# Kernel optimization log

Hardware: AMD Instinct MI355X
Metric: run time of the kernel (lower is better)

The kernel has to match this reference:

```python
import jax, jax.numpy as jnp
import numpy as np

N_U = 16        # walkers per molecule
N_ORB = 12      # number of orbitals
N_FEAT = 14     # feature dim, fixed by w being 14x14
H1_THR = 0.0
H2_THR = 0.0


def setup_inputs() -> dict:
    key = jax.random.key(0)
    k1, k2, k3, k4, k5 = jax.random.split(key, 5)
    B = 16
    T = B * N_U  # 256 total walker samples
    mfv = jax.random.normal(k1, (T, N_ORB, N_FEAT), jnp.float32) * 0.1
    h1 = jax.random.normal(k2, (T, N_ORB, N_ORB), jnp.float32)
    h2 = jax.random.normal(k3, (T, N_ORB, N_ORB, N_ORB, N_ORB), jnp.float32)
    # occupancies in {1,2} so p_x_i determinants are generically nonzero
    V_n_hf = 1 + jax.random.randint(k4, (B, N_U, N_ORB), 0, 2, jnp.int32)
    w = jax.random.normal(k5, (N_FEAT, N_FEAT), jnp.float32) * 0.1
    return {"molec_feature_vectors": mfv, "h1": h1, "h2": h2,
            "V_n_hf": V_n_hf, "w": w}


def _forward(mfv, h1, h2, V_n_hf, w):
    T, n, f = mfv.shape
    B = T // N_U
    Vn = V_n_hf.reshape(T, n)                      # (T, n_orb) int occupancies

    eye = jnp.eye(n, dtype=jnp.int32)
    # c^dag c excitation patterns: (n, n^2)
    c1 = (eye[:, None, :] - eye[:, :, None]).reshape(n, n * n)
    # c^dag c^dag c c patterns: (n, n^4)
    c2 = (c1[:, None, :] - c1[:, :, None]).reshape(n, n ** 4)
    Wsym = w + w.T
    h1f = h1.reshape(T, n * n)
    h2f = h2.reshape(T, n ** 4)

    def per_sample(x, h1v, h2v, phi):
        # G[a,i] = phi[a] @ Wsym @ phi[i]; the c-sum inside calc_ampl factors as
        # det( G * (S S^T) ) because einsum('abc,bj,ijc->aic') keeps c aligned.
        G = phi @ Wsym @ phi.T                     # (n, n)

        # ---- one-body term ----
        s1 = c1 + x[:, None]                       # (n, n^2)
        m1 = ((s1.max(0) - s1.min(0)) == 1) & (h1v > H1_THR)
        s1f = s1.astype(phi.dtype) * m1            # boolean_mask -> zero columns
        det1 = jnp.linalg.det(G * (s1f @ s1f.T))
        e1 = det1 ** 2 * jnp.sum(jnp.where(m1, h1v, 0.0) ** 2)

        # ---- two-body term ----
        s2 = c2 + x[:, None]                       # (n, n^4)
        m2 = ((s2.max(0) - s2.min(0)) == 1) & (h2v > H2_THR)
        s2f = s2.astype(phi.dtype) * m2
        # reduce_sum over (orbital, feature) of phi[:, :, None] * s2[:, None, :]
        a2 = phi.sum(1) @ s2f                      # (n^4,)
        e2 = jnp.sum((jnp.where(m2, h2v, 0.0) * a2) ** 2)

        # ---- sampling probability of current state ----
        xf = x.astype(phi.dtype)
        p = jnp.linalg.det(G * jnp.outer(xf, xf)) ** 2
        return e1 + e2, p

    e, p = jax.vmap(per_sample)(Vn, h1f, h2f, mfv)
    e = e.reshape(B, N_U)
    p = p.reshape(B, N_U)
    return jnp.sum(e * p, axis=1) / jnp.sum(p, axis=1)   # (B,)


def reference(molec_feature_vectors, h1, h2, V_n_hf, w):
    return _forward(molec_feature_vectors, h1, h2, V_n_hf, w)
```

## Files before the change

kernel.cpp:

```cpp
#include <hip/hip_runtime.h>

#define NORB   12
#define NFEAT  14
#define NCOL1  144
#define NCOL2  20736
#define RPB    192
#define NSPLIT 9
#define CPS    (NSPLIT + 1)
#define NT     256
#define WPS    (NSPLIT * 3)

extern "C" __global__ void __launch_bounds__(RPB)
eloc_fused(const float* __restrict__ mfv, const float* __restrict__ h1,
           const float* __restrict__ h2, const int* __restrict__ vn,
           const float* __restrict__ w,
           double* __restrict__ ep, double* __restrict__ part)
{
    const int tid = threadIdx.x;
    const int bid = blockIdx.x;
    const int t   = bid / CPS;
    const int ch  = bid % CPS;

    __shared__ float phi_s[NORB][NFEAT];
    __shared__ int   x_s[NORB];
    __shared__ float W_s[NFEAT][NFEAT];
    __shared__ float tmp_s[NORB][NFEAT];
    __shared__ float G_s[NORB][NORB];
    __shared__ unsigned char m1_s[NCOL1];
    __shared__ int Ri_s[NORB], Rj_s[NORB], M_s;
    __shared__ double A1[NORB][NORB], A2[NORB][NORB];
    __shared__ double red_s[RPB / 64];
    __shared__ double det_s[2];
    __shared__ double h1sum_s;

    if (ch != 0) {
        const int lane = tid & 63, wvi = tid >> 6;
        const int r = (ch - 1) * RPB + tid;
        const int i = r / 144, j = (r / NORB) % NORB, p = r % NORB;

        const float4* hr = (const float4*)(h2 + (size_t)t * NCOL2 + (size_t)r * NORB);
        const float4 ha = hr[0], hb = hr[1], hc = hr[2];

        int   xv  = 1;
        float psl = 0.f;
        if (lane < NORB) {
            xv = vn[t * NORB + lane];
            const float* pr = mfv + (size_t)t * NORB * NFEAT + lane * NFEAT;
            float s = 0.f;
            #pragma unroll
            for (int f = 0; f < NFEAT; ++f) s += pr[f];
            psl = s;
        }
        const unsigned long long bal = __ballot(xv == 2);
        const int X2  = (int)(bal & 0xFFFull);
        const int nx2 = ~X2 & 0xFFF;

        float sv = (lane < NORB) ? psl * (float)xv : 0.f;
        sv += __shfl_xor(sv, 8, 16);
        sv += __shfl_xor(sv, 4, 16);
        sv += __shfl_xor(sv, 2, 16);
        sv += __shfl_xor(sv, 1, 16);
        const float Sv = __shfl(sv, 0, 64);

        float psv[NORB];
        #pragma unroll
        for (int q = 0; q < NORB; ++q) psv[q] = __shfl(psl, q, 64);

        const int bi = 1 << i, bj = 1 << j, bp = 1 << p;
        const int um0 = 0xFFF & ~(bi | bj | bp);
        const int xi = 1 + ((X2 >> i) & 1);
        const int xj = 1 + ((X2 >> j) & 1);
        const int xp = 1 + ((X2 >> p) & 1);
        const int basei = xi + 1 - ((bi >> j) & 1) - ((bi >> p) & 1);
        const int basej = xj + ((bj >> i) & 1) - 1 - ((bj >> p) & 1);
        const int basep = xp + ((bp >> i) & 1) - ((bp >> j) & 1) - 1;
        const float a2b = Sv + __shfl(psl, i, 64) - __shfl(psl, j, 64)
                        - __shfl(psl, p, 64);

        float acc = 0.f;
#define COLQ(q, hv) {                                                       \
        const int bq  = 1 << (q);                                           \
        const int um  = um0 & ~bq;                                          \
        const int hm1 = nx2 & um, hm2 = X2 & um;                            \
        int mn = hm1 ? 1 : (hm2 ? 2 : 9);                                   \
        int mx = hm2 ? 2 : (hm1 ? 1 : -9);                                  \
        const int iq = (bi >> (q)) & 1, jq = (bj >> (q)) & 1,               \
                  pq = (bp >> (q)) & 1;                                     \
        const int vi = basei + iq, vj = basej + jq, vp = basep + pq;        \
        const int xq = 1 + ((X2 >> (q)) & 1);                               \
        const int vq = xq + 1 + iq - jq - pq;                               \
        mn = min(min(mn, vi), min(vj, min(vp, vq)));                        \
        mx = max(max(mx, vi), max(vj, max(vp, vq)));                        \
        const bool ok = (mx - mn == 1) && ((hv) > 0.0f);                    \
        const float tq = ok ? (hv) * (a2b + psv[q]) : 0.0f;                 \
        acc = fmaf(tq, tq, acc);                                            \
    }
        COLQ(0,  ha.x)  COLQ(1,  ha.y)  COLQ(2,  ha.z)  COLQ(3,  ha.w)
        COLQ(4,  hb.x)  COLQ(5,  hb.y)  COLQ(6,  hb.z)  COLQ(7,  hb.w)
        COLQ(8,  hc.x)  COLQ(9,  hc.y)  COLQ(10, hc.z)  COLQ(11, hc.w)
#undef COLQ

        double accd = (double)acc;
        #pragma unroll
        for (int o = 32; o > 0; o >>= 1) accd += __shfl_down(accd, o, 64);
        if (lane == 0) part[t * WPS + (ch - 1) * 3 + wvi] = accd;
    } else {
        if (tid < NORB * NFEAT)
            phi_s[tid / NFEAT][tid % NFEAT] = mfv[(size_t)t * NORB * NFEAT + tid];
        if (tid >= NORB * NFEAT && tid < NORB * NFEAT + NORB)
            x_s[tid - NORB * NFEAT] = vn[t * NORB + (tid - NORB * NFEAT)];
        for (int k2 = tid; k2 < NFEAT * NFEAT; k2 += RPB) {
            int r2 = k2 / NFEAT, c2 = k2 % NFEAT;
            W_s[r2][c2] = w[k2] + w[c2 * NFEAT + r2];
        }
        __syncthreads();

        int X2 = 0;
        #pragma unroll
        for (int a = 0; a < NORB; ++a) X2 |= (x_s[a] == 2) ? (1 << a) : 0;
        const int nx2 = ~X2 & 0xFFF;

        if (tid < NORB * NFEAT) {
            int a = tid / NFEAT, f = tid % NFEAT;
            float s = 0.f;
            #pragma unroll
            for (int g = 0; g < NFEAT; ++g) s += phi_s[a][g] * W_s[g][f];
            tmp_s[a][f] = s;
        }
        __syncthreads();
        if (tid < NCOL1) {
            int a = tid / NORB, i = tid % NORB;
            float s = 0.f;
            #pragma unroll
            for (int f = 0; f < NFEAT; ++f) s += tmp_s[a][f] * phi_s[i][f];
            G_s[a][i] = s;
        }

        double h1c = 0.0;
        if (tid < NCOL1) {
            int ii = tid / NORB, jj = tid % NORB;
            int um  = 0xFFF & ~((1 << ii) | (1 << jj));
            int hm1 = nx2 & um, hm2 = X2 & um;
            int mn = hm1 ? 1 : (hm2 ? 2 : 9);
            int mx = hm2 ? 2 : (hm1 ? 1 : -9);
            int d  = (ii == jj) ? 0 : 1;
            int vi = x_s[ii] - d, vj = x_s[jj] + d;
            mn = min(mn, min(vi, vj));
            mx = max(mx, max(vi, vj));
            float h1v = h1[(size_t)t * NCOL1 + tid];
            bool ok = (mx - mn == 1) && (h1v > 0.0f);
            m1_s[tid] = ok ? 1 : 0;
            if (ok) h1c = (double)h1v * (double)h1v;
        }
        __syncthreads();
        {
            #pragma unroll
            for (int o = 32; o > 0; o >>= 1) h1c += __shfl_down(h1c, o, 64);
            const int wvv = tid >> 6, lane = tid & 63;
            if (lane == 0) red_s[wvv] = h1c;
            __syncthreads();
            if (tid == 0) h1sum_s = red_s[0] + red_s[1] + red_s[2];
        }

        if (tid < NORB) {
            int ri = 0, rj = 0;
            #pragma unroll
            for (int o = 0; o < NORB; ++o) {
                ri += m1_s[tid * NORB + o];
                rj += m1_s[o * NORB + tid];
            }
            Ri_s[tid] = ri;
            Rj_s[tid] = rj;
        }
        __syncthreads();
        if (tid == 0) {
            int m = 0;
            #pragma unroll
            for (int o = 0; o < NORB; ++o) m += Ri_s[o];
            M_s = m;
        }
        __syncthreads();

        if (tid < NCOL1) {
            int a = tid / NORB, b = tid % NORB;
            int xa = x_s[a], xb = x_s[b];
            int Da = Rj_s[a] - Ri_s[a], Db = Rj_s[b] - Ri_s[b];
            int s1 = xa * xb * M_s + xa * Db + xb * Da
                   - (int)m1_s[b * NORB + a] - (int)m1_s[a * NORB + b];
            if (a == b) s1 += Rj_s[a] + Ri_s[a];
            A1[a][b] = (double)G_s[a][b] * (double)s1;
            A2[a][b] = (double)G_s[a][b];
        }
        __syncthreads();

        const int wvv = tid >> 6, lane = tid & 63;
        if (wvv < 2) {
            const double* Abase = (wvv == 0) ? &A1[0][0] : &A2[0][0];
            const int rl = (lane < NORB) ? lane : 0;
            double a[NORB];
            #pragma unroll
            for (int c = 0; c < NORB; ++c) a[c] = Abase[rl * NORB + c];
            double det = 1.0;
            #pragma unroll
            for (int k = 0; k < NORB; ++k) {
                double key = (lane >= k && lane < NORB) ? fabs(a[k]) : -1.0;
                int idx = lane;
                #pragma unroll
                for (int off = 8; off >= 1; off >>= 1) {
                    double k2 = __shfl_xor(key, off);
                    int    i2 = __shfl_xor(idx, off);
                    if (k2 > key || (k2 == key && i2 < idx)) { key = k2; idx = i2; }
                }
                int pr = idx;
                if (pr != k) det = -det;
                int src = (lane == k) ? pr : ((lane == pr) ? k : lane);
                #pragma unroll
                for (int c = 0; c < NORB; ++c) a[c] = __shfl(a[c], src);
                double pk[NORB];
                #pragma unroll
                for (int c = 0; c < NORB; ++c) pk[c] = __shfl(a[c], k);
                double piv = pk[k];
                det *= piv;
                double inv = (piv != 0.0) ? 1.0 / piv : 0.0;
                double f = (lane > k && lane < NORB) ? a[k] * inv : 0.0;
                #pragma unroll
                for (int c = 0; c < NORB; ++c) a[c] = fma(-f, pk[c], a[c]);
            }
            if (lane == 0) det_s[wvv] = det;
        }
        __syncthreads();

        if (tid == 0) {
            double e1 = det_s[0] * det_s[0] * h1sum_s;
            int n2 = __popc(X2);
            double pd = det_s[1] * (double)(1ull << (2 * n2));
            ep[2 * t]     = e1;
            ep[2 * t + 1] = pd * pd;
        }
    }
}

extern "C" __global__ void __launch_bounds__(256)
eloc_final(const double* __restrict__ ep, const double* __restrict__ part,
           float* __restrict__ out)
{
    const int s = threadIdx.x;
    __shared__ double se_s[NT], sp_s[NT];
    if (s < NT) {
        double e2 = 0.0;
        #pragma unroll
        for (int k = 0; k < WPS; ++k) e2 += part[s * WPS + k];
        double e = ep[2 * s] + e2;
        double p = ep[2 * s + 1];
        se_s[s] = e * p;
        sp_s[s] = p;
    }
    __syncthreads();
    if (s < NT / 16) {
        double se = 0.0, sp = 0.0;
        #pragma unroll
        for (int u = 0; u < 16; ++u) {
            se += se_s[s * 16 + u];
            sp += sp_s[s * 16 + u];
        }
        out[s] = (float)(se / sp);
    }
}

extern "C" void kernel_launch(void* const* d_in, const int* in_sizes, int n_in,
                              void* d_out, int out_size, void* d_ws, size_t ws_size,
                              hipStream_t stream) {
    const float* mfv = (const float*)d_in[0];
    const float* h1  = (const float*)d_in[1];
    const float* h2  = (const float*)d_in[2];
    const int*   vn  = (const int*)d_in[3];
    const float* w   = (const float*)d_in[4];
    float* out = (float*)d_out;

    double* ep   = (double*)d_ws;
    double* part = ep + 2 * NT;

    hipLaunchKernelGGL(eloc_fused, dim3(NT * CPS), dim3(RPB), 0, stream,
                       mfv, h1, h2, vn, w, ep, part);
    hipLaunchKernelGGL(eloc_final, dim3(1), dim3(256), 0, stream, ep, part, out);
}
```

Measured before the change: 25.19 us.

## Fuse final reduction into main kernel via atomics and last-block counter

Merges the separate final-reduction kernel into the main kernel. Per-wave partial sums go into a per-sample double via atomicAdd, and a global atomic counter lets the last block to finish compute the per-molecule ratios. This removes one kernel launch and its dependency gap, but adds a memset of the workspace, atomic contention on 256 accumulators, and relaxed-ordering memory semantics that rely on an explicit vmcnt wait for visibility.

Measured after the change: 56.15 us. +123.0%, slower.

```diff
diff --git a/kernel.cpp b/kernel.cpp
--- a/kernel.cpp
+++ b/kernel.cpp
@@ -8,13 +8,14 @@
 #define NSPLIT 9
 #define CPS    (NSPLIT + 1)
 #define NT     256
-#define WPS    (NSPLIT * 3)
+#define GRID   (NT * CPS)
 
 extern "C" __global__ void __launch_bounds__(RPB)
-eloc_fused(const float* __restrict__ mfv, const float* __restrict__ h1,
-           const float* __restrict__ h2, const int* __restrict__ vn,
-           const float* __restrict__ w,
-           double* __restrict__ ep, double* __restrict__ part)
+eloc_one(const float* __restrict__ mfv, const float* __restrict__ h1,
+         const float* __restrict__ h2, const int* __restrict__ vn,
+         const float* __restrict__ w,
+         double* __restrict__ ep, double* __restrict__ e2acc,
+         unsigned* __restrict__ ctr, float* __restrict__ out)
 {
     const int tid = threadIdx.x;
     const int bid = blockIdx.x;
@@ -32,9 +33,11 @@
     __shared__ double red_s[RPB / 64];
     __shared__ double det_s[2];
     __shared__ double h1sum_s;
+    __shared__ double se_s[NT], sp_s[NT];
+    __shared__ int last_s;
 
     if (ch != 0) {
-        const int lane = tid & 63, wvi = tid >> 6;
+        const int lane = tid & 63;
         const int r = (ch - 1) * RPB + tid;
         const int i = r / 144, j = (r / NORB) % NORB, p = r % NORB;
 
@@ -103,7 +106,7 @@
         double accd = (double)acc;
         #pragma unroll
         for (int o = 32; o > 0; o >>= 1) accd += __shfl_down(accd, o, 64);
-        if (lane == 0) part[t * WPS + (ch - 1) * 3 + wvi] = accd;
+        if (lane == 0) atomicAdd(&e2acc[t], accd);
     } else {
         if (tid < NORB * NFEAT)
             phi_s[tid / NFEAT][tid % NFEAT] = mfv[(size_t)t * NORB * NFEAT + tid];
@@ -234,36 +237,41 @@
             double e1 = det_s[0] * det_s[0] * h1sum_s;
             int n2 = __popc(X2);
             double pd = det_s[1] * (double)(1ull << (2 * n2));
-            ep[2 * t]     = e1;
-            ep[2 * t + 1] = pd * pd;
-        }
-    }
-}
-
-extern "C" __global__ void __launch_bounds__(256)
-eloc_final(const double* __restrict__ ep, const double* __restrict__ part,
-           float* __restrict__ out)
-{
-    const int s = threadIdx.x;
-    __shared__ double se_s[NT], sp_s[NT];
-    if (s < NT) {
-        double e2 = 0.0;
-        #pragma unroll
-        for (int k = 0; k < WPS; ++k) e2 += part[s * WPS + k];
-        double e = ep[2 * s] + e2;
-        double p = ep[2 * s + 1];
-        se_s[s] = e * p;
-        sp_s[s] = p;
-    }
+            __hip_atomic_store(&ep[2 * t], e1, __ATOMIC_RELAXED, __HIP_MEMORY_SCOPE_AGENT);
+            __hip_atomic_store(&ep[2 * t + 1], pd * pd, __ATOMIC_RELAXED, __HIP_MEMORY_SCOPE_AGENT);
+        }
+    }
+
+    asm volatile("s_waitcnt vmcnt(0)" ::: "memory");
     __syncthreads();
-    if (s < NT / 16) {
-        double se = 0.0, sp = 0.0;
-        #pragma unroll
-        for (int u = 0; u < 16; ++u) {
-            se += se_s[s * 16 + u];
-            sp += sp_s[s * 16 + u];
-        }
-        out[s] = (float)(se / sp);
+    if (tid == 0) {
+        unsigned old = __hip_atomic_fetch_add(ctr, 1u, __ATOMIC_RELAXED,
+                                              __HIP_MEMORY_SCOPE_AGENT);
+        last_s = (old == (unsigned)(GRID - 1)) ? 1 : 0;
+    }
+    __syncthreads();
+    if (last_s) {
+        for (int s2 = tid; s2 < NT; s2 += RPB) {
+            double e2 = __hip_atomic_load(&e2acc[s2], __ATOMIC_RELAXED,
+                                          __HIP_MEMORY_SCOPE_AGENT);
+            double e1 = __hip_atomic_load(&ep[2 * s2], __ATOMIC_RELAXED,
+                                          __HIP_MEMORY_SCOPE_AGENT);
+            double p  = __hip_atomic_load(&ep[2 * s2 + 1], __ATOMIC_RELAXED,
+                                          __HIP_MEMORY_SCOPE_AGENT);
+            double e = e1 + e2;
+            se_s[s2] = e * p;
+            sp_s[s2] = p;
+        }
+        __syncthreads();
+        if (tid < NT / 16) {
+            double se = 0.0, sp = 0.0;
+            #pragma unroll
+            for (int u = 0; u < 16; ++u) {
+                se += se_s[tid * 16 + u];
+                sp += sp_s[tid * 16 + u];
+            }
+            out[tid] = (float)(se / sp);
+        }
     }
 }
 
@@ -277,10 +285,11 @@
     const float* w   = (const float*)d_in[4];
     float* out = (float*)d_out;
 
-    double* ep   = (double*)d_ws;
-    double* part = ep + 2 * NT;
-
-    hipLaunchKernelGGL(eloc_fused, dim3(NT * CPS), dim3(RPB), 0, stream,
-                       mfv, h1, h2, vn, w, ep, part);
-    hipLaunchKernelGGL(eloc_final, dim3(1), dim3(256), 0, stream, ep, part, out);
+    unsigned* ctr   = (unsigned*)d_ws;
+    double*   e2acc = (double*)((char*)d_ws + 8);
+    double*   ep    = (double*)((char*)d_ws + 4096);
+
+    hipMemsetAsync(d_ws, 0, 8 + NT * 8, stream);
+    hipLaunchKernelGGL(eloc_one, dim3(GRID), dim3(RPB), 0, stream,
+                       mfv, h1, h2, vn, w, ep, e2acc, ctr, out);
 }
```
